# Kernel tuning notes

Hardware: AMD Instinct MI355X
Metric: run time of the kernel (lower is better)

## Reference

```python
import jax, jax.numpy as jnp
import numpy as np

N_UNITS = 512
N_HEADS = 8
CHUNK = N_UNITS // N_HEADS
SCALE = 1.0 / (CHUNK ** 0.5)


def setup_inputs() -> dict:
    key = jax.random.key(0)
    k1, k2, k3, k4, k5, k6 = jax.random.split(key, 6)
    B, Nx, Ny = 8, 1024, 1024
    x = jax.random.normal(k1, (B, N_UNITS, Nx), dtype=jnp.float32)
    y = jax.random.normal(k2, (B, N_UNITS, Ny), dtype=jnp.float32)
    xy_mask = jax.random.randint(k3, (B, Nx, Ny), 0, 2) > 0
    # conv1x1 weight [out, in] (ConvolutionSentence, bias=False)
    W = jax.random.normal(k4, (N_UNITS, N_UNITS), dtype=jnp.float32) * (1.0 / np.sqrt(N_UNITS))
    fc_w = jax.random.normal(k5, (1, N_HEADS), dtype=jnp.float32) * (1.0 / np.sqrt(N_HEADS))
    fc_b = jax.random.normal(k6, (1,), dtype=jnp.float32) * 0.01
    return {"x": x, "y": y, "xy_mask": xy_mask, "W": W, "fc_w": fc_w, "fc_b": fc_b}


def reference(x, y, xy_mask, W, fc_w, fc_b):
    B, U, Nx = x.shape
    Ny = y.shape[2]
    H, C = N_HEADS, CHUNK
    # 1x1 conv over channel dim == linear on channels
    _x = jnp.einsum('oi,bin->bon', W, x)  # [B, U, Nx]
    _y = jnp.einsum('oi,bim->bom', W, y)  # [B, U, Ny]
    # split channels into heads (contiguous chunks, matching torch.split)
    xh = _x.reshape(B, H, C, Nx)
    yh = _y.reshape(B, H, C, Ny)
    # per-head scores: relu, then scale, then mask (order matches torch code)
    s = jnp.einsum('bhcn,bhcm->bhnm', xh, yh)  # [B, H, Nx, Ny]
    s = jnp.maximum(s, 0.0) * SCALE
    s = jnp.where(xy_mask[:, None, :, :], s, 0.0)
    similarity = s.sum(axis=(2, 3))  # [B, H]
    n_el = xy_mask.sum(axis=(1, 2))
    n_el = jnp.where(n_el == 0, 1, n_el).astype(similarity.dtype)
    expectation = similarity / n_el[:, None]
    return expectation @ fc_w.T + fc_b  # [B, 1]
```

## Files before the change

kernel.cpp:

```cpp
#include <hip/hip_runtime.h>
#include <stdint.h>

#define UU 512
#define NHEAD 8
#define NB 8
#define NXX 1024
#define NYY 1024
#define SCALE_F 0.125f

typedef __bf16 bf16x8 __attribute__((ext_vector_type(8)));
typedef float f32x4 __attribute__((ext_vector_type(4)));
typedef unsigned short us4 __attribute__((ext_vector_type(4)));

__device__ __forceinline__ unsigned short f2bf(float f) {
  union { float f; uint32_t u; } v; v.f = f;
  return (unsigned short)((v.u + 0x7FFFu + ((v.u >> 16) & 1u)) >> 16);
}

__global__ void detect_mask(const unsigned char* __restrict__ m, int* __restrict__ det) {
  int t = threadIdx.x;
  int c1 = 0;
  for (int q = t; q < 16384; q += 256) c1 |= m[q * 4 + 1];
  if (c1) atomicOr(&det[0], 1);
}

__global__ void prep_kernel(const float* __restrict__ W, unsigned short* __restrict__ Wp,
                            const void* __restrict__ maskp, const int* __restrict__ det,
                            unsigned long long* __restrict__ mb) {
  __shared__ unsigned short sm[256];
  int blk = blockIdx.x, t = threadIdx.x;
  if (blk < 128) {
    int s = blk * 256 + t;
    int ub = s >> 10, kb = (s >> 6) & 15, l = s & 63;
    int u = ub * 16 + (l & 15), k = kb * 32 + (l >> 4) * 8;
    const float* src = W + (size_t)u * UU + k;
    float4 a = *(const float4*)src;
    float4 bq = *(const float4*)(src + 4);
    uint4 o;
    o.x = (unsigned)f2bf(a.x) | ((unsigned)f2bf(a.y) << 16);
    o.y = (unsigned)f2bf(a.z) | ((unsigned)f2bf(a.w) << 16);
    o.z = (unsigned)f2bf(bq.x) | ((unsigned)f2bf(bq.y) << 16);
    o.w = (unsigned)f2bf(bq.z) | ((unsigned)f2bf(bq.w) << 16);
    *(uint4*)(Wp + (size_t)s * 8) = o;
    return;
  }
  int pb = blk - 128;
  size_t g = (size_t)pb * 256 + t;
  unsigned int bm = 0;
  if (det[0]) {
    uint4 v = *(const uint4*)((const unsigned char*)maskp + g * 16);
    unsigned int wd[4] = {v.x, v.y, v.z, v.w};
#pragma unroll
    for (int j = 0; j < 16; j++)
      bm |= (((wd[j >> 2] >> ((j & 3) * 8)) & 0xffu) != 0u) << j;
  } else {
    const unsigned int* mp = (const unsigned int*)maskp + g * 16;
#pragma unroll
    for (int q = 0; q < 4; q++) {
      uint4 v = *(const uint4*)(mp + q * 4);
      unsigned int wd[4] = {v.x, v.y, v.z, v.w};
#pragma unroll
      for (int j = 0; j < 4; j++)
        bm |= (wd[j] != 0u) << (q * 4 + j);
    }
  }
  sm[t] = (unsigned short)bm;
  __syncthreads();
  if (t < 64) {
    unsigned long long w0 = sm[t * 4], w1 = sm[t * 4 + 1], w2 = sm[t * 4 + 2], w3 = sm[t * 4 + 3];
    mb[(size_t)pb * 64 + t] = w0 | (w1 << 16) | (w2 << 32) | (w3 << 48);
  }
}

__global__ __launch_bounds__(256, 2) void conv_fused(
    const float* __restrict__ x, const float* __restrict__ y,
    const unsigned short* __restrict__ Wp, unsigned short* __restrict__ pc) {
  __shared__ unsigned short xs[64 * 512];
  int fl = blockIdx.x;
  int bz = fl & 15, nt = (fl >> 4) & 15, ut = fl >> 8;
  int b = bz & 7;
  const float* src = (bz >> 3) ? y : x;
  int n0 = nt * 64;
  int t = threadIdx.x, w = t >> 6, l = t & 63;
  int lane_m = l & 15, lane_g = l >> 4;

  {
    int cq = (t & 15) * 4;
    int i2b = (t >> 4) * 2;
    const float* gb = src + (size_t)b * UU * NXX + n0 + cq;
#pragma unroll
    for (int it = 0; it < 16; it++) {
      int i2 = i2b + it * 32;
      float4 va = *(const float4*)(gb + (size_t)i2 * NXX);
      float4 vb = *(const float4*)(gb + (size_t)(i2 + 1) * NXX);
      float fa[4] = {va.x, va.y, va.z, va.w};
      float fb[4] = {vb.x, vb.y, vb.z, vb.w};
#pragma unroll
      for (int j = 0; j < 4; j++) {
        int n = cq + j;
        unsigned int pk = (unsigned)f2bf(fa[j]) | ((unsigned)f2bf(fb[j]) << 16);
        int e = n * 512 + (i2 ^ ((n & 7) << 3));
        *(unsigned int*)&xs[e] = pk;
      }
    }
  }
  __syncthreads();

  int u0 = ut * 256 + w * 64;
  int ub0 = u0 >> 4;
  const unsigned short* wb0 = Wp + (size_t)l * 8;
  f32x4 acc[4][4] = {};
  bf16x8 aA[4], aB[4], bA[4], bB[4];

#define LOADW(Adst, Bdst, KB) do {                                            \
    _Pragma("unroll") for (int tu = 0; tu < 4; tu++)                          \
      Adst[tu] = *(const bf16x8*)(wb0 + ((size_t)(ub0 + tu) * 16 + (KB)) * 512); \
    _Pragma("unroll") for (int tn = 0; tn < 4; tn++) {                        \
      int nl_ = tn * 16 + lane_m;                                             \
      int ka_ = (KB) * 32 + lane_g * 8;                                       \
      Bdst[tn] = *(const bf16x8*)&xs[nl_ * 512 + (ka_ ^ ((nl_ & 7) << 3))];   \
    }                                                                         \
  } while (0)
#define DOMFMA(Ab, Bb) do {                                                   \
    _Pragma("unroll") for (int tn = 0; tn < 4; tn++)                          \
    _Pragma("unroll") for (int tu = 0; tu < 4; tu++)                          \
      acc[tn][tu] = __builtin_amdgcn_mfma_f32_16x16x32_bf16(Ab[tu], Bb[tn], acc[tn][tu], 0, 0, 0); \
  } while (0)

  LOADW(aA, bA, 0);
#pragma unroll
  for (int kp = 0; kp < 8; kp++) {
    LOADW(aB, bB, 2 * kp + 1);
    DOMFMA(aA, bA);
    if (kp < 7) LOADW(aA, bA, 2 * kp + 2);
    DOMFMA(aB, bB);
  }
#undef LOADW
#undef DOMFMA

  unsigned short* ob = pc + (size_t)bz * 64 * 8 * 2 * 512;
  int h = u0 >> 6;
  int e0 = 4 * (lane_g & 1);
#pragma unroll
  for (int tn = 0; tn < 4; tn++)
#pragma unroll
    for (int tu = 0; tu < 4; tu++) {
      int q16 = nt * 4 + tn;
      int kb = tu >> 1;
      int g = (2 * tu + (lane_g >> 1)) & 3;
      size_t slot = ((size_t)q16 * 8 + h) * 2 + kb;
      us4 pk;
      pk.x = f2bf(acc[tn][tu][0]); pk.y = f2bf(acc[tn][tu][1]);
      pk.z = f2bf(acc[tn][tu][2]); pk.w = f2bf(acc[tn][tu][3]);
      *(us4*)(ob + slot * 512 + (g * 16 + lane_m) * 8 + e0) = pk;
    }
}

__global__ __launch_bounds__(256, 4) void score_kernel(
    const unsigned short* __restrict__ pc, const unsigned long long* __restrict__ mb,
    float* __restrict__ part) {
  __shared__ unsigned long long msk[64];
  __shared__ float red[4][8];
  int fl = blockIdx.x;
  int b = fl & 7, rr = fl >> 3;
  int nt = rr & 15, mt = rr >> 4;
  int t = threadIdx.x, w = t >> 6, l = t & 63;
  int lane_m = l & 15, lane_g = l >> 4;
  int n0 = nt * 64, m0 = mt * 64;
  int nw0 = (w & 1) * 32, hq = (w >> 1) * 4;

  if (t < 64) msk[t] = mb[((size_t)b * NXX + n0 + t) * 16 + mt];
  __syncthreads();

  if (w == 0) {
    unsigned long long mv = msk[l];
    unsigned int cl = (unsigned int)__popcll(mv);
    for (int s = 1; s < 64; s <<= 1) cl += __shfl_xor(cl, s);
    if (l == 0) red[0][4] = (float)cl;
  } else if (l == 0) {
    red[w][4] = 0.f;
  }

  unsigned long long mw[2][4];
#pragma unroll
  for (int tn = 0; tn < 2; tn++)
#pragma unroll
    for (int r = 0; r < 4; r++)
      mw[tn][r] = msk[nw0 + tn * 16 + 4 * lane_g + r] >> lane_m;

  int xq0 = (n0 + nw0) >> 4;
  int yq0 = m0 >> 4;
  const unsigned short* xpl = pc + ((size_t)b * 64) * 8 * 2 * 512 + (size_t)l * 8;
  const unsigned short* ypl = pc + ((size_t)(NB + b) * 64) * 8 * 2 * 512 + (size_t)l * 8;
  float hsv[4] = {0.f, 0.f, 0.f, 0.f};
#pragma unroll
  for (int hh = 0; hh < 4; hh++) {
    int h = hq + hh;
    bf16x8 afr[2][2], bfr[4][2];
#pragma unroll
    for (int tn = 0; tn < 2; tn++)
#pragma unroll
      for (int kb = 0; kb < 2; kb++)
        afr[tn][kb] = *(const bf16x8*)(xpl + ((((size_t)(xq0 + tn)) * 8 + h) * 2 + kb) * 512);
#pragma unroll
    for (int tm = 0; tm < 4; tm++)
#pragma unroll
      for (int kb = 0; kb < 2; kb++)
        bfr[tm][kb] = *(const bf16x8*)(ypl + ((((size_t)(yq0 + tm)) * 8 + h) * 2 + kb) * 512);
#pragma unroll
    for (int tn = 0; tn < 2; tn++)
#pragma unroll
      for (int tm = 0; tm < 4; tm++) {
        f32x4 acc = {};
        acc = __builtin_amdgcn_mfma_f32_16x16x32_bf16(afr[tn][0], bfr[tm][0], acc, 0, 0, 0);
        acc = __builtin_amdgcn_mfma_f32_16x16x32_bf16(afr[tn][1], bfr[tm][1], acc, 0, 0, 0);
#pragma unroll
        for (int r = 0; r < 4; r++) {
          float v = acc[r];
          v = v > 0.f ? v : 0.f;
          unsigned int bit = (unsigned int)(mw[tn][r] >> (tm * 16)) & 1u;
          hsv[hh] += bit ? v : 0.f;
        }
      }
  }
#pragma unroll
  for (int hh = 0; hh < 4; hh++) {
    float hs = hsv[hh];
    for (int s = 1; s < 64; s <<= 1) hs += __shfl_xor(hs, s);
    if (l == 0) red[w][hh] = hs;
  }
  __syncthreads();
  float* pb = part + (size_t)fl * 16;
  if (t < 8) {
    int q = t >> 2, hh = t & 3;
    pb[t] = red[q * 2][hh] + red[q * 2 + 1][hh];
  } else if (t == 8) {
    pb[8] = red[0][4] + red[1][4] + red[2][4] + red[3][4];
  }
}

__global__ __launch_bounds__(256) void finalize(
    const float* __restrict__ part, const float* __restrict__ fcw,
    const float* __restrict__ fcb, float* __restrict__ out) {
  __shared__ float red[4][9];
  int b = blockIdx.x;
  int t = threadIdx.x, w = t >> 6, l = t & 63;
  const float* pb = part + (size_t)(t * 8 + b) * 16;
  float v[9];
#pragma unroll
  for (int j = 0; j < 9; j++) v[j] = pb[j];
#pragma unroll
  for (int j = 0; j < 9; j++) {
    float s = v[j];
    for (int ss = 1; ss < 64; ss <<= 1) s += __shfl_xor(s, ss);
    v[j] = s;
  }
  if (l == 0)
#pragma unroll
    for (int j = 0; j < 9; j++) red[w][j] = v[j];
  __syncthreads();
  if (t == 0) {
    float s = 0.f, cn = 0.f;
#pragma unroll
    for (int h = 0; h < NHEAD; h++)
      s += (red[0][h] + red[1][h] + red[2][h] + red[3][h]) * fcw[h];
    cn = red[0][8] + red[1][8] + red[2][8] + red[3][8];
    if (cn < 0.5f) cn = 1.f;
    out[b] = s * (SCALE_F / cn) + fcb[0];
  }
}

extern "C" void kernel_launch(void* const* d_in, const int* in_sizes, int n_in,
                              void* d_out, int out_size, void* d_ws, size_t ws_size,
                              hipStream_t stream) {
  const float* x = (const float*)d_in[0];
  const float* y = (const float*)d_in[1];
  const void* mask = d_in[2];
  const float* W = (const float*)d_in[3];
  const float* fcw = (const float*)d_in[4];
  const float* fcb = (const float*)d_in[5];
  float* out = (float*)d_out;
  char* ws = (char*)d_ws;

  unsigned short* pc = (unsigned short*)ws;
  unsigned short* Wp = (unsigned short*)(ws + (16u << 20));
  float* part = (float*)(ws + (16u << 20) + (512u << 10));
  unsigned long long* mb = (unsigned long long*)(ws + (16u << 20) + (640u << 10));
  int* det = (int*)(ws + (16u << 20) + (1664u << 10));

  hipMemsetAsync(det, 0, 64, stream);
  detect_mask<<<1, 256, 0, stream>>>((const unsigned char*)mask, det);
  prep_kernel<<<2176, 256, 0, stream>>>(W, Wp, mask, det, mb);
  conv_fused<<<512, 256, 0, stream>>>(x, y, Wp, pc);
  score_kernel<<<2048, 256, 0, stream>>>(pc, mb, part);
  finalize<<<NB, 256, 0, stream>>>(part, fcw, fcb, out);
}
```

Before: 145.6 us.

## Fuse y-projection into score kernel and transpose mask bitmap layout

New measurement: 152.2 us. 1.05x slower.

```diff
diff --git a/kernel.cpp b/kernel.cpp
--- a/kernel.cpp
+++ b/kernel.cpp
@@ -26,7 +26,7 @@
 
 __global__ void prep_kernel(const float* __restrict__ W, unsigned short* __restrict__ Wp,
                             const void* __restrict__ maskp, const int* __restrict__ det,
-                            unsigned long long* __restrict__ mb) {
+                            unsigned int* __restrict__ mbt) {
   __shared__ unsigned short sm[256];
   int blk = blockIdx.x, t = threadIdx.x;
   if (blk < 128) {
@@ -66,20 +66,22 @@
   }
   sm[t] = (unsigned short)bm;
   __syncthreads();
-  if (t < 64) {
-    unsigned long long w0 = sm[t * 4], w1 = sm[t * 4 + 1], w2 = sm[t * 4 + 2], w3 = sm[t * 4 + 3];
-    mb[(size_t)pb * 64 + t] = w0 | (w1 << 16) | (w2 << 32) | (w3 << 48);
-  }
-}
-
-__global__ __launch_bounds__(256, 2) void conv_fused(
-    const float* __restrict__ x, const float* __restrict__ y,
-    const unsigned short* __restrict__ Wp, unsigned short* __restrict__ pc) {
+  if (t < 128) {
+    int row = t >> 5, mt = t & 31;
+    unsigned int w32 = (unsigned)sm[row * 64 + mt * 2]
+                     | ((unsigned)sm[row * 64 + mt * 2 + 1] << 16);
+    int gr = pb * 4 + row;
+    int b = gr >> 10, n = gr & 1023;
+    mbt[(((size_t)b * 32 + mt) << 10) + n] = w32;
+  }
+}
+
+__global__ __launch_bounds__(256, 2) void conv_x(
+    const float* __restrict__ x, const unsigned short* __restrict__ Wp,
+    unsigned short* __restrict__ pcx) {
   __shared__ unsigned short xs[64 * 512];
   int fl = blockIdx.x;
-  int bz = fl & 15, nt = (fl >> 4) & 15, ut = fl >> 8;
-  int b = bz & 7;
-  const float* src = (bz >> 3) ? y : x;
+  int b = fl & 7, nt = (fl >> 3) & 15, ut = fl >> 7;
   int n0 = nt * 64;
   int t = threadIdx.x, w = t >> 6, l = t & 63;
   int lane_m = l & 15, lane_g = l >> 4;
@@ -87,7 +89,7 @@
   {
     int cq = (t & 15) * 4;
     int i2b = (t >> 4) * 2;
-    const float* gb = src + (size_t)b * UU * NXX + n0 + cq;
+    const float* gb = x + (size_t)b * UU * NXX + n0 + cq;
 #pragma unroll
     for (int it = 0; it < 16; it++) {
       int i2 = i2b + it * 32;
@@ -138,7 +140,7 @@
 #undef LOADW
 #undef DOMFMA
 
-  unsigned short* ob = pc + (size_t)bz * 64 * 8 * 2 * 512;
+  unsigned short* ob = pcx + (size_t)b * 64 * 8 * 2 * 512;
   int h = u0 >> 6;
   int e0 = 4 * (lane_g & 1);
 #pragma unroll
@@ -156,115 +158,177 @@
     }
 }
 
-__global__ __launch_bounds__(256, 4) void score_kernel(
-    const unsigned short* __restrict__ pc, const unsigned long long* __restrict__ mb,
+__global__ __launch_bounds__(256, 2) void conv_score(
+    const float* __restrict__ y, const unsigned short* __restrict__ Wp,
+    const unsigned short* __restrict__ pcx, const unsigned int* __restrict__ mbt,
     float* __restrict__ part) {
-  __shared__ unsigned long long msk[64];
-  __shared__ float red[4][8];
+  __shared__ unsigned short yin[32 * 512];
+  __shared__ unsigned short yfr[32 * 512];
+  __shared__ unsigned int mrow[1024];
+  __shared__ float red[4][4];
   int fl = blockIdx.x;
-  int b = fl & 7, rr = fl >> 3;
-  int nt = rr & 15, mt = rr >> 4;
+  int b = fl & 7, mt = fl >> 3;
+  int m0 = mt * 32;
   int t = threadIdx.x, w = t >> 6, l = t & 63;
   int lane_m = l & 15, lane_g = l >> 4;
-  int n0 = nt * 64, m0 = mt * 64;
-  int nw0 = (w & 1) * 32, hq = (w >> 1) * 4;
-
-  if (t < 64) msk[t] = mb[((size_t)b * NXX + n0 + t) * 16 + mt];
-  __syncthreads();
-
-  if (w == 0) {
-    unsigned long long mv = msk[l];
-    unsigned int cl = (unsigned int)__popcll(mv);
-    for (int s = 1; s < 64; s <<= 1) cl += __shfl_xor(cl, s);
-    if (l == 0) red[0][4] = (float)cl;
-  } else if (l == 0) {
-    red[w][4] = 0.f;
-  }
-
-  unsigned long long mw[2][4];
-#pragma unroll
-  for (int tn = 0; tn < 2; tn++)
-#pragma unroll
-    for (int r = 0; r < 4; r++)
-      mw[tn][r] = msk[nw0 + tn * 16 + 4 * lane_g + r] >> lane_m;
-
-  int xq0 = (n0 + nw0) >> 4;
-  int yq0 = m0 >> 4;
-  const unsigned short* xpl = pc + ((size_t)b * 64) * 8 * 2 * 512 + (size_t)l * 8;
-  const unsigned short* ypl = pc + ((size_t)(NB + b) * 64) * 8 * 2 * 512 + (size_t)l * 8;
-  float hsv[4] = {0.f, 0.f, 0.f, 0.f};
-#pragma unroll
-  for (int hh = 0; hh < 4; hh++) {
-    int h = hq + hh;
-    bf16x8 afr[2][2], bfr[4][2];
+
+  {
+    int cq = (t & 7) * 4;
+    int i2b = (t >> 3) * 2;
+    const float* gb = y + (size_t)b * UU * NXX + m0 + cq;
+#pragma unroll
+    for (int it = 0; it < 8; it++) {
+      int i2 = i2b + it * 64;
+      float4 va = *(const float4*)(gb + (size_t)i2 * NXX);
+      float4 vb = *(const float4*)(gb + (size_t)(i2 + 1) * NXX);
+      float fa[4] = {va.x, va.y, va.z, va.w};
+      float fb[4] = {vb.x, vb.y, vb.z, vb.w};
+#pragma unroll
+      for (int j = 0; j < 4; j++) {
+        int n = cq + j;
+        unsigned int pk = (unsigned)f2bf(fa[j]) | ((unsigned)f2bf(fb[j]) << 16);
+        int e = n * 512 + (i2 ^ ((n & 7) << 3));
+        *(unsigned int*)&yin[e] = pk;
+      }
+    }
+  }
+  unsigned int cl;
+  {
+    uint4 mv = *(const uint4*)(mbt + (((size_t)b * 32 + mt) << 10) + t * 4);
+    *(uint4*)&mrow[t * 4] = mv;
+    cl = __popc(mv.x) + __popc(mv.y) + __popc(mv.z) + __popc(mv.w);
+  }
+  for (int s = 1; s < 64; s <<= 1) cl += __shfl_xor(cl, s);
+  if (l == 0) red[w][2] = (float)cl;
+  __syncthreads();
+
+  const unsigned short* wb0 = Wp + (size_t)l * 8;
+#pragma unroll
+  for (int half = 0; half < 2; half++) {
+    int ub0 = w * 8 + half * 4;
+    f32x4 acc[2][4] = {};
+    bf16x8 aA[4], aB[4], bA[2], bB[2];
+#define LOADW2(Adst, Bdst, KB) do {                                           \
+    _Pragma("unroll") for (int tu = 0; tu < 4; tu++)                          \
+      Adst[tu] = *(const bf16x8*)(wb0 + ((size_t)(ub0 + tu) * 16 + (KB)) * 512); \
+    _Pragma("unroll") for (int tn = 0; tn < 2; tn++) {                        \
+      int nl_ = tn * 16 + lane_m;                                             \
+      int ka_ = (KB) * 32 + lane_g * 8;                                       \
+      Bdst[tn] = *(const bf16x8*)&yin[nl_ * 512 + (ka_ ^ ((nl_ & 7) << 3))];  \
+    }                                                                         \
+  } while (0)
+#define DOMFMA2(Ab, Bb) do {                                                  \
+    _Pragma("unroll") for (int tn = 0; tn < 2; tn++)                          \
+    _Pragma("unroll") for (int tu = 0; tu < 4; tu++)                          \
+      acc[tn][tu] = __builtin_amdgcn_mfma_f32_16x16x32_bf16(Ab[tu], Bb[tn], acc[tn][tu], 0, 0, 0); \
+  } while (0)
+    LOADW2(aA, bA, 0);
+#pragma unroll
+    for (int kp = 0; kp < 8; kp++) {
+      LOADW2(aB, bB, 2 * kp + 1);
+      DOMFMA2(aA, bA);
+      if (kp < 7) LOADW2(aA, bA, 2 * kp + 2);
+      DOMFMA2(aB, bB);
+    }
+#undef LOADW2
+#undef DOMFMA2
+    int h = w * 2 + half;
+    int e0 = 4 * (lane_g & 1);
 #pragma unroll
     for (int tn = 0; tn < 2; tn++)
 #pragma unroll
-      for (int kb = 0; kb < 2; kb++)
-        afr[tn][kb] = *(const bf16x8*)(xpl + ((((size_t)(xq0 + tn)) * 8 + h) * 2 + kb) * 512);
-#pragma unroll
-    for (int tm = 0; tm < 4; tm++)
-#pragma unroll
-      for (int kb = 0; kb < 2; kb++)
-        bfr[tm][kb] = *(const bf16x8*)(ypl + ((((size_t)(yq0 + tm)) * 8 + h) * 2 + kb) * 512);
-#pragma unroll
-    for (int tn = 0; tn < 2; tn++)
-#pragma unroll
-      for (int tm = 0; tm < 4; tm++) {
-        f32x4 acc = {};
-        acc = __builtin_amdgcn_mfma_f32_16x16x32_bf16(afr[tn][0], bfr[tm][0], acc, 0, 0, 0);
-        acc = __builtin_amdgcn_mfma_f32_16x16x32_bf16(afr[tn][1], bfr[tm][1], acc, 0, 0, 0);
-#pragma unroll
-        for (int r = 0; r < 4; r++) {
-          float v = acc[r];
-          v = v > 0.f ? v : 0.f;
-          unsigned int bit = (unsigned int)(mw[tn][r] >> (tm * 16)) & 1u;
-          hsv[hh] += bit ? v : 0.f;
+      for (int tu = 0; tu < 4; tu++) {
+        int kb = tu >> 1;
+        int g = (2 * tu + (lane_g >> 1)) & 3;
+        int slot = (tn * 8 + h) * 2 + kb;
+        us4 pk;
+        pk.x = f2bf(acc[tn][tu][0]); pk.y = f2bf(acc[tn][tu][1]);
+        pk.z = f2bf(acc[tn][tu][2]); pk.w = f2bf(acc[tn][tu][3]);
+        *(us4*)&yfr[slot * 512 + (g * 16 + lane_m) * 8 + e0] = pk;
+      }
+  }
+  __syncthreads();
+
+  int h0 = w * 2;
+  bf16x8 bfr[2][2][2];
+#pragma unroll
+  for (int hh = 0; hh < 2; hh++)
+#pragma unroll
+    for (int tm = 0; tm < 2; tm++)
+#pragma unroll
+      for (int kb = 0; kb < 2; kb++) {
+        int slot = (tm * 8 + h0 + hh) * 2 + kb;
+        bfr[hh][tm][kb] = *(const bf16x8*)&yfr[slot * 512 + l * 8];
+      }
+  const unsigned short* xpl = pcx + (size_t)b * 64 * 8 * 2 * 512 + (size_t)l * 8;
+  float hsv[2] = {0.f, 0.f};
+  for (int nt = 0; nt < 16; nt++) {
+    bf16x8 afr[2][4][2];
+#pragma unroll
+    for (int hh = 0; hh < 2; hh++)
+#pragma unroll
+      for (int tn = 0; tn < 4; tn++)
+#pragma unroll
+        for (int kb = 0; kb < 2; kb++)
+          afr[hh][tn][kb] = *(const bf16x8*)(xpl +
+              ((((size_t)(nt * 4 + tn)) * 8 + h0 + hh) * 2 + kb) * 512);
+    unsigned int mwv[4][4];
+#pragma unroll
+    for (int tn = 0; tn < 4; tn++)
+#pragma unroll
+      for (int r = 0; r < 4; r++)
+        mwv[tn][r] = mrow[nt * 64 + tn * 16 + 4 * lane_g + r] >> lane_m;
+#pragma unroll
+    for (int hh = 0; hh < 2; hh++)
+#pragma unroll
+      for (int tn = 0; tn < 4; tn++)
+#pragma unroll
+        for (int tm = 0; tm < 2; tm++) {
+          f32x4 acc = {};
+          acc = __builtin_amdgcn_mfma_f32_16x16x32_bf16(afr[hh][tn][0], bfr[hh][tm][0], acc, 0, 0, 0);
+          acc = __builtin_amdgcn_mfma_f32_16x16x32_bf16(afr[hh][tn][1], bfr[hh][tm][1], acc, 0, 0, 0);
+#pragma unroll
+          for (int r = 0; r < 4; r++) {
+            float v = acc[r];
+            v = v > 0.f ? v : 0.f;
+            hsv[hh] += ((mwv[tn][r] >> (tm * 16)) & 1u) ? v : 0.f;
+          }
         }
-      }
-  }
-#pragma unroll
-  for (int hh = 0; hh < 4; hh++) {
+  }
+#pragma unroll
+  for (int hh = 0; hh < 2; hh++) {
     float hs = hsv[hh];
     for (int s = 1; s < 64; s <<= 1) hs += __shfl_xor(hs, s);
     if (l == 0) red[w][hh] = hs;
   }
   __syncthreads();
   float* pb = part + (size_t)fl * 16;
-  if (t < 8) {
-    int q = t >> 2, hh = t & 3;
-    pb[t] = red[q * 2][hh] + red[q * 2 + 1][hh];
-  } else if (t == 8) {
-    pb[8] = red[0][4] + red[1][4] + red[2][4] + red[3][4];
-  }
-}
-
-__global__ __launch_bounds__(256) void finalize(
-    const float* __restrict__ part, const float* __restrict__ fcw,
-    const float* __restrict__ fcb, float* __restrict__ out) {
-  __shared__ float red[4][9];
-  int b = blockIdx.x;
-  int t = threadIdx.x, w = t >> 6, l = t & 63;
-  const float* pb = part + (size_t)(t * 8 + b) * 16;
+  if (t < 8) pb[t] = red[t >> 1][t & 1];
+  else if (t == 8) pb[8] = red[0][2] + red[1][2] + red[2][2] + red[3][2];
+}
+
+__global__ void finalize(const float* __restrict__ part, const float* __restrict__ fcw,
+                         const float* __restrict__ fcb, float* __restrict__ out) {
+  int b = blockIdx.x, t = threadIdx.x;
   float v[9];
 #pragma unroll
-  for (int j = 0; j < 9; j++) v[j] = pb[j];
+  for (int j = 0; j < 9; j++) v[j] = 0.f;
+  if (t < 32) {
+    const float* pb = part + (size_t)(t * 8 + b) * 16;
+#pragma unroll
+    for (int j = 0; j < 9; j++) v[j] = pb[j];
+  }
 #pragma unroll
   for (int j = 0; j < 9; j++) {
     float s = v[j];
     for (int ss = 1; ss < 64; ss <<= 1) s += __shfl_xor(s, ss);
     v[j] = s;
   }
-  if (l == 0)
-#pragma unroll
-    for (int j = 0; j < 9; j++) red[w][j] = v[j];
-  __syncthreads();
   if (t == 0) {
-    float s = 0.f, cn = 0.f;
-#pragma unroll
-    for (int h = 0; h < NHEAD; h++)
-      s += (red[0][h] + red[1][h] + red[2][h] + red[3][h]) * fcw[h];
-    cn = red[0][8] + red[1][8] + red[2][8] + red[3][8];
+    float s = 0.f;
+#pragma unroll
+    for (int h = 0; h < NHEAD; h++) s += v[h] * fcw[h];
+    float cn = v[8];
     if (cn < 0.5f) cn = 1.f;
     out[b] = s * (SCALE_F / cn) + fcb[0];
   }
@@ -282,16 +346,16 @@
   float* out = (float*)d_out;
   char* ws = (char*)d_ws;
 
-  unsigned short* pc = (unsigned short*)ws;
-  unsigned short* Wp = (unsigned short*)(ws + (16u << 20));
-  float* part = (float*)(ws + (16u << 20) + (512u << 10));
-  unsigned long long* mb = (unsigned long long*)(ws + (16u << 20) + (640u << 10));
-  int* det = (int*)(ws + (16u << 20) + (1664u << 10));
+  unsigned short* pcx = (unsigned short*)ws;
+  unsigned short* Wp = (unsigned short*)(ws + (8u << 20));
+  unsigned int* mbt = (unsigned int*)(ws + (8u << 20) + (512u << 10));
+  float* part = (float*)(ws + (8u << 20) + (1536u << 10));
+  int* det = (int*)(ws + (8u << 20) + (1552u << 10));
 
   hipMemsetAsync(det, 0, 64, stream);
   detect_mask<<<1, 256, 0, stream>>>((const unsigned char*)mask, det);
-  prep_kernel<<<2176, 256, 0, stream>>>(W, Wp, mask, det, mb);
-  conv_fused<<<512, 256, 0, stream>>>(x, y, Wp, pc);
-  score_kernel<<<2048, 256, 0, stream>>>(pc, mb, part);
-  finalize<<<NB, 256, 0, stream>>>(part, fcw, fcb, out);
-}
+  prep_kernel<<<2176, 256, 0, stream>>>(W, Wp, mask, det, mbt);
+  conv_x<<<256, 256, 0, stream>>>(x, Wp, pcx);
+  conv_score<<<256, 256, 0, stream>>>(y, Wp, pcx, mbt, part);
+  finalize<<<NB, 64, 0, stream>>>(part, fcw, fcb, out);
+}
```
